# Kernel tuning notes

Measured on AMD Instinct MI355X. Metric: run time of the kernel, lower is better.

Reference implementation:

```python
import jax, jax.numpy as jnp
import numpy as np

N, IN_CH, HID, HEADS, NCLS, E = 50000, 128, 32, 8, 16, 800000
NEG_SLOPE = 0.2  # PyG GATConv default negative_slope


def setup_inputs() -> dict:
    key = jax.random.key(0)
    ks = jax.random.split(key, 10)
    sc = lambda fan: 1.0 / np.sqrt(fan).astype(np.float32)
    x = jax.random.normal(ks[0], (N, IN_CH), jnp.float32)
    edge_index = jax.random.randint(ks[1], (2, E), 0, N, jnp.int32)
    W1 = jax.random.normal(ks[2], (IN_CH, HEADS * HID), jnp.float32) * sc(IN_CH)
    att_src1 = jax.random.normal(ks[3], (HEADS, HID), jnp.float32) * sc(HID)
    att_dst1 = jax.random.normal(ks[4], (HEADS, HID), jnp.float32) * sc(HID)
    b1 = jnp.zeros((HEADS * HID,), jnp.float32)
    W2 = jax.random.normal(ks[5], (HEADS * HID, NCLS), jnp.float32) * sc(HEADS * HID)
    att_src2 = jax.random.normal(ks[6], (1, NCLS), jnp.float32) * sc(NCLS)
    att_dst2 = jax.random.normal(ks[7], (1, NCLS), jnp.float32) * sc(NCLS)
    b2 = jnp.zeros((NCLS,), jnp.float32)
    return {"x": x, "edge_index": edge_index, "W1": W1, "att_src1": att_src1,
            "att_dst1": att_dst1, "b1": b1, "W2": W2, "att_src2": att_src2,
            "att_dst2": att_dst2, "b2": b2}


def _gat_layer(x, W, a_src, a_dst, src, dst, heads, ch):
    """PyG GATConv core: per-edge LeakyReLU attention, scatter-softmax over
    destination neighborhoods, scatter-add aggregation. Returns [N, heads, ch]."""
    n = x.shape[0]
    h = (x @ W).reshape(n, heads, ch)                      # [N,H,C]
    e_src = jnp.einsum('nhc,hc->nh', h, a_src)             # [N,H]
    e_dst = jnp.einsum('nhc,hc->nh', h, a_dst)             # [N,H]
    e = jax.nn.leaky_relu(e_src[src] + e_dst[dst], NEG_SLOPE)  # [Etot,H]
    # scatter-softmax grouped by destination node (self-loops ensure nonempty)
    m = jax.ops.segment_max(e, dst, num_segments=n)        # [N,H]
    p = jnp.exp(e - m[dst])
    denom = jax.ops.segment_sum(p, dst, num_segments=n)    # [N,H]
    alpha = p / denom[dst]                                 # [Etot,H]
    out = jax.ops.segment_sum(alpha[:, :, None] * h[src], dst, num_segments=n)
    return out                                             # [N,H,C]


def reference(x, edge_index, W1, att_src1, att_dst1, b1, W2, att_src2, att_dst2, b2):
    n = x.shape[0]
    loops = jnp.arange(n, dtype=edge_index.dtype)          # add_self_loops=True
    src = jnp.concatenate([edge_index[0], loops])
    dst = jnp.concatenate([edge_index[1], loops])
    # conv1: heads=8, concat=True
    h1 = _gat_layer(x, W1, att_src1, att_dst1, src, dst, HEADS, HID)
    h1 = h1.reshape(n, HEADS * HID) + b1
    h1 = jax.nn.elu(h1)  # dropout is identity in eval mode
    # conv2: heads=1, concat=False (mean over 1 head == that head)
    h2 = _gat_layer(h1, W2, att_src2, att_dst2, src, dst, 1, NCLS)
    return h2[:, 0, :] + b2
```

## Files before the change

### kernel.cpp

```cpp
#include <hip/hip_runtime.h>
#include <hip/hip_bf16.h>


#define IN_CH 128
#define HIDC  256
#define NCLS  16
#define NEG_SLOPE 0.2f

typedef short bf16x8 __attribute__((ext_vector_type(8)));
typedef float f32x4 __attribute__((ext_vector_type(4)));

__device__ __forceinline__ unsigned int f2bf(float f) {
    unsigned int u = __float_as_uint(f);
    return (u + 0x7fffu + ((u >> 16) & 1u)) >> 16;
}
__device__ __forceinline__ float bf_lo(unsigned int w) { return __uint_as_float(w << 16); }
__device__ __forceinline__ float bf_hi(unsigned int w) { return __uint_as_float(w & 0xffff0000u); }


__global__ void count_fill_kernel(const int* __restrict__ ei, int* __restrict__ counts,
                                  int* __restrict__ erank, int E, int Etot,
                                  int* __restrict__ colB, int fill_n, int dummyB,
                                  unsigned short* __restrict__ Hb, float* __restrict__ ES1,
                                  float* __restrict__ H2, float* __restrict__ ES2,
                                  const float* __restrict__ W1,
                                  unsigned short* __restrict__ W1t, int N) {
    int i = blockIdx.x * blockDim.x + threadIdx.x;
    if (i < Etot) {
        int dst = (i < E) ? ei[E + i] : (i - E);
        erank[i] = atomicAdd(&counts[dst], 1);
    }
    if (i < fill_n) colB[i] = dummyB;
    if (i < IN_CH * HIDC) {
        int c = i >> 7, k = i & 127;
        W1t[i] = (unsigned short)f2bf(W1[k * HIDC + c]);
    }
    if (i < HIDC) Hb[(size_t)N * HIDC + i] = 0;
    if (i < NCLS) H2[(size_t)N * NCLS + i] = 0.f;
    if (i < 8) ES1[(size_t)N * 8 + i] = -3.0e38f;
    if (i == 0) ES2[N] = -3.0e38f;
}


__global__ __launch_bounds__(256) void scanA_kernel(const int* __restrict__ counts,
                                                    int* __restrict__ row_start,
                                                    int* __restrict__ bsums, int n) {
    __shared__ int wsum[4];
    int tid = threadIdx.x, lane = tid & 63, wid = tid >> 6;
    int i = blockIdx.x * 256 + tid;
    int v = (i < n) ? ((counts[i] + 3) & ~3) : 0;
    int x = v;
    #pragma unroll
    for (int off = 1; off < 64; off <<= 1) {
        int t = __shfl_up(x, off);
        if (lane >= off) x += t;
    }
    if (lane == 63) wsum[wid] = x;
    __syncthreads();
    if (tid < 4) {
        int w = wsum[tid];
        #pragma unroll
        for (int off = 1; off < 4; off <<= 1) {
            int t = __shfl_up(w, off);
            if (tid >= off) w += t;
        }
        wsum[tid] = w;
    }
    __syncthreads();
    int wex = wid ? wsum[wid - 1] : 0;
    if (i < n) row_start[i] = wex + (x - v);
    if (tid == 255) bsums[blockIdx.x] = wsum[3];
}

__global__ __launch_bounds__(256) void scanB_kernel(const int* __restrict__ bsums,
                                                    int* __restrict__ bofs,
                                                    int* __restrict__ row_start,
                                                    int nb, int n) {
    __shared__ int wsum[4];
    int tid = threadIdx.x, lane = tid & 63, wid = tid >> 6;
    int v = (tid < nb) ? bsums[tid] : 0;
    int x = v;
    #pragma unroll
    for (int off = 1; off < 64; off <<= 1) {
        int t = __shfl_up(x, off);
        if (lane >= off) x += t;
    }
    if (lane == 63) wsum[wid] = x;
    __syncthreads();
    if (tid < 4) {
        int w = wsum[tid];
        #pragma unroll
        for (int off = 1; off < 4; off <<= 1) {
            int t = __shfl_up(w, off);
            if (tid >= off) w += t;
        }
        wsum[tid] = w;
    }
    __syncthreads();
    int wex = wid ? wsum[wid - 1] : 0;
    if (tid < nb) bofs[tid] = wex + (x - v);
    if (tid == nb - 1) row_start[n] = wex + x;
}

__global__ __launch_bounds__(256) void scanC_kernel(int* __restrict__ row_start,
                                                    const int* __restrict__ bofs, int n) {
    int i = blockIdx.x * 256 + threadIdx.x;
    if (i < n) row_start[i] += bofs[blockIdx.x];
}

__global__ void scatter_kernel(const int* __restrict__ ei, const int* __restrict__ row_start,
                               const int* __restrict__ erank, int* __restrict__ colB,
                               int E, int Etot) {
    int e = blockIdx.x * blockDim.x + threadIdx.x;
    if (e >= Etot) return;
    int src, dst;
    if (e < E) { src = ei[e]; dst = ei[E + e]; }
    else       { src = e - E; dst = e - E; }
    colB[row_start[dst] + erank[e]] = src * (HIDC * 2);
}


#define LDK 72

__global__ __launch_bounds__(256) void gemm1_mfma(const float* __restrict__ A,
                                                  const unsigned short* __restrict__ W1t,
                                                  const float* __restrict__ a_src,
                                                  const float* __restrict__ a_dst,
                                                  unsigned short* __restrict__ Hb,
                                                  float* __restrict__ ES,
                                                  float* __restrict__ ED, int M) {
    __shared__ unsigned short As[128 * LDK];
    __shared__ unsigned short Bs[128 * LDK];
    int tid = threadIdx.x;
    int row0 = blockIdx.x * 128, col0 = blockIdx.y * 128;
    int lane = tid & 63, wid = tid >> 6;
    int wr = wid >> 1, wc = wid & 1;
    int la = lane & 15, lg = lane >> 4;
    f32x4 acc[4][4] = {};

    int r = tid >> 1, hf = tid & 1;
    int gr = row0 + r;
    bool okA = gr < M;
    const float4* asrc = reinterpret_cast<const float4*>(A + (size_t)(okA ? gr : 0) * IN_CH) + hf * 8;
    const uint4*  bsrc = reinterpret_cast<const uint4*>(W1t + (size_t)(col0 + r) * IN_CH) + hf * 4;
    unsigned short* adst = &As[r * LDK + hf * 32];
    unsigned short* bdst = &Bs[r * LDK + hf * 32];

    #pragma unroll
    for (int kt = 0; kt < 2; ++kt) {
        #pragma unroll
        for (int it = 0; it < 8; ++it) {
            float4 v = okA ? asrc[it] : make_float4(0.f, 0.f, 0.f, 0.f);
            uint2 w;
            w.x = f2bf(v.x) | (f2bf(v.y) << 16);
            w.y = f2bf(v.z) | (f2bf(v.w) << 16);
            *reinterpret_cast<uint2*>(adst + it * 4) = w;
        }
        #pragma unroll
        for (int it = 0; it < 4; ++it) {
            uint4 v = bsrc[it];
            *reinterpret_cast<uint4*>(bdst + it * 8) = v;
        }
        asrc += 16;
        bsrc += 8;
        __syncthreads();
        #pragma unroll
        for (int k0 = 0; k0 < 64; k0 += 32) {
            bf16x8 af[4], bfr[4];
            #pragma unroll
            for (int m = 0; m < 4; ++m)
                af[m] = *reinterpret_cast<const bf16x8*>(&As[(wr * 64 + m * 16 + la) * LDK + k0 + lg * 8]);
            #pragma unroll
            for (int n2 = 0; n2 < 4; ++n2)
                bfr[n2] = *reinterpret_cast<const bf16x8*>(&Bs[(wc * 64 + n2 * 16 + la) * LDK + k0 + lg * 8]);
            #pragma unroll
            for (int m = 0; m < 4; ++m) {
                #pragma unroll
                for (int n2 = 0; n2 < 4; ++n2)
                    acc[m][n2] = __builtin_amdgcn_mfma_f32_16x16x32_bf16(af[m], bfr[n2], acc[m][n2], 0, 0, 0);
            }
        }
        __syncthreads();
    }

    #pragma unroll
    for (int m = 0; m < 4; ++m) {
        #pragma unroll
        for (int j = 0; j < 4; ++j) {
            int grow = row0 + wr * 64 + m * 16 + lg * 4 + j;
            if (grow < M) {
                int gcol = col0 + wc * 64 + la;
                #pragma unroll
                for (int n2 = 0; n2 < 4; ++n2)
                    Hb[(size_t)grow * HIDC + gcol + n2 * 16] = (unsigned short)f2bf(acc[m][n2][j]);
            }
        }
    }

    int h0 = (col0 + wc * 64) >> 5;
    float as00 = a_src[h0 * 32 + la],        as01 = a_src[h0 * 32 + 16 + la];
    float ad00 = a_dst[h0 * 32 + la],        ad01 = a_dst[h0 * 32 + 16 + la];
    float as10 = a_src[(h0 + 1) * 32 + la],  as11 = a_src[(h0 + 1) * 32 + 16 + la];
    float ad10 = a_dst[(h0 + 1) * 32 + la],  ad11 = a_dst[(h0 + 1) * 32 + 16 + la];
    #pragma unroll
    for (int m = 0; m < 4; ++m) {
        #pragma unroll
        for (int j = 0; j < 4; ++j) {
            float v0 = acc[m][0][j], v1 = acc[m][1][j];
            float v2 = acc[m][2][j], v3 = acc[m][3][j];
            float es0 = v0 * as00 + v1 * as01;
            float ed0 = v0 * ad00 + v1 * ad01;
            float es1 = v2 * as10 + v3 * as11;
            float ed1 = v2 * ad10 + v3 * ad11;
            #pragma unroll
            for (int off = 1; off < 16; off <<= 1) {
                es0 += __shfl_xor(es0, off);
                ed0 += __shfl_xor(ed0, off);
                es1 += __shfl_xor(es1, off);
                ed1 += __shfl_xor(ed1, off);
            }
            int grow = row0 + wr * 64 + m * 16 + lg * 4 + j;
            if (la == 0 && grow < M) {
                ES[grow * 8 + h0] = es0;
                ED[grow * 8 + h0] = ed0;
                ES[grow * 8 + h0 + 1] = es1;
                ED[grow * 8 + h0 + 1] = ed1;
            }
        }
    }
}


#define EDGE4(cbv)                                                              \
    {                                                                           \
        float e0 = *(const float*)(ESb + (((cbv).x >> 4) | hoff));              \
        float e1 = *(const float*)(ESb + (((cbv).y >> 4) | hoff));              \
        float e2 = *(const float*)(ESb + (((cbv).z >> 4) | hoff));              \
        float e3 = *(const float*)(ESb + (((cbv).w >> 4) | hoff));              \
        uint2 v0 = *(const uint2*)(Hbb + ((cbv).x + lane8));                    \
        uint2 v1 = *(const uint2*)(Hbb + ((cbv).y + lane8));                    \
        uint2 v2 = *(const uint2*)(Hbb + ((cbv).z + lane8));                    \
        uint2 v3 = *(const uint2*)(Hbb + ((cbv).w + lane8));                    \
        e0 += ed; e1 += ed; e2 += ed; e3 += ed;                                 \
        e0 = fmaxf(e0, NEG_SLOPE * e0);                                         \
        e1 = fmaxf(e1, NEG_SLOPE * e1);                                         \
        e2 = fmaxf(e2, NEG_SLOPE * e2);                                         \
        e3 = fmaxf(e3, NEG_SLOPE * e3);                                         \
        float p0 = __expf(e0), p1 = __expf(e1), p2 = __expf(e2), p3 = __expf(e3);\
        s += (p0 + p1) + (p2 + p3);                                             \
        acc.x = fmaf(p0, bf_lo(v0.x), acc.x);                                   \
        acc.y = fmaf(p0, bf_hi(v0.x), acc.y);                                   \
        acc.z = fmaf(p0, bf_lo(v0.y), acc.z);                                   \
        acc.w = fmaf(p0, bf_hi(v0.y), acc.w);                                   \
        acc.x = fmaf(p1, bf_lo(v1.x), acc.x);                                   \
        acc.y = fmaf(p1, bf_hi(v1.x), acc.y);                                   \
        acc.z = fmaf(p1, bf_lo(v1.y), acc.z);                                   \
        acc.w = fmaf(p1, bf_hi(v1.y), acc.w);                                   \
        acc.x = fmaf(p2, bf_lo(v2.x), acc.x);                                   \
        acc.y = fmaf(p2, bf_hi(v2.x), acc.y);                                   \
        acc.z = fmaf(p2, bf_lo(v2.y), acc.z);                                   \
        acc.w = fmaf(p2, bf_hi(v2.y), acc.w);                                   \
        acc.x = fmaf(p3, bf_lo(v3.x), acc.x);                                   \
        acc.y = fmaf(p3, bf_hi(v3.x), acc.y);                                   \
        acc.z = fmaf(p3, bf_lo(v3.y), acc.z);                                   \
        acc.w = fmaf(p3, bf_hi(v3.y), acc.w);                                   \
    }

__global__ __launch_bounds__(256) void agg1_kernel(const unsigned short* __restrict__ Hb,
                                                   const float* __restrict__ ES,
                                                   const float* __restrict__ ED,
                                                   const int* __restrict__ row_start,
                                                   const int* __restrict__ colB,
                                                   const float* __restrict__ b1,
                                                   const float* __restrict__ W2,
                                                   const float* __restrict__ as2,
                                                   const float* __restrict__ ad2,
                                                   float* __restrict__ H2,
                                                   float* __restrict__ ES2,
                                                   float* __restrict__ ED2, int N) {
    __shared__ float W2t[16][260];
    __shared__ float h1row[4][260];
    int tid = threadIdx.x;
    #pragma unroll
    for (int it = 0; it < 16; ++it) {
        int idx = tid + it * 256;
        int c = idx & 15, k = idx >> 4;
        W2t[c][k + (k >> 6)] = W2[idx];
    }
    __syncthreads();

    int n = blockIdx.x * 4 + (tid >> 6);
    if (n >= N) return;
    int lane = tid & 63;
    int wv = tid >> 6;
    int h = lane >> 3;
    unsigned int hoff = h << 2;
    unsigned int lane8 = lane << 3;
    int s0 = row_start[n], s1 = row_start[n + 1];
    float ed = ED[n * 8 + h];
    const char* ESb = (const char*)ES;
    const char* Hbb = (const char*)Hb;

    float s = 0.f;
    float4 acc = make_float4(0.f, 0.f, 0.f, 0.f);

    int i = s0;
    for (; i + 7 < s1; i += 8) {
        uint4 cbA = *reinterpret_cast<const uint4*>(&colB[i]);
        uint4 cbB = *reinterpret_cast<const uint4*>(&colB[i + 4]);
        EDGE4(cbA);
        EDGE4(cbB);
    }
    if (i < s1) {
        uint4 cb = *reinterpret_cast<const uint4*>(&colB[i]);
        EDGE4(cb);
    }

    float inv = 1.0f / s;
    const float4 bv = *reinterpret_cast<const float4*>(&b1[lane * 4]);
    float4 o;
    o.x = acc.x * inv + bv.x;
    o.y = acc.y * inv + bv.y;
    o.z = acc.z * inv + bv.z;
    o.w = acc.w * inv + bv.w;
    o.x = o.x > 0.f ? o.x : expm1f(o.x);
    o.y = o.y > 0.f ? o.y : expm1f(o.y);
    o.z = o.z > 0.f ? o.z : expm1f(o.z);
    o.w = o.w > 0.f ? o.w : expm1f(o.w);

    {
        float* hr = &h1row[wv][0];
        int base = lane * 4 + (lane >> 4);
        hr[base + 0] = o.x;
        hr[base + 1] = o.y;
        hr[base + 2] = o.z;
        hr[base + 3] = o.w;
        __builtin_amdgcn_wave_barrier();
        int kg = lane >> 4, c = lane & 15;
        const float* wcol = &W2t[c][kg * 65];
        const float* hseg = &hr[kg * 65];
        float p = 0.f;
        #pragma unroll 16
        for (int k = 0; k < 64; ++k) p = fmaf(hseg[k], wcol[k], p);
        p += __shfl_xor(p, 16);
        p += __shfl_xor(p, 32);
        if (kg == 0) H2[(size_t)n * NCLS + c] = p;
        float es = p * as2[c];
        float edv = p * ad2[c];
        #pragma unroll
        for (int off = 1; off < 16; off <<= 1) {
            es += __shfl_xor(es, off);
            edv += __shfl_xor(edv, off);
        }
        if (lane == 0) {
            ES2[n] = es;
            ED2[n] = edv;
        }
    }
}


__global__ __launch_bounds__(256) void agg2_kernel(const float* __restrict__ H2,
                                                   const float* __restrict__ ES,
                                                   const float* __restrict__ ED,
                                                   const int* __restrict__ row_start,
                                                   const int* __restrict__ colB,
                                                   const float* __restrict__ b2,
                                                   float* __restrict__ out, int N) {
    int g = blockIdx.x * 4 + (threadIdx.x >> 6);
    if (g >= N) return;
    int lane = threadIdx.x & 63;
    int ep = lane >> 4;
    unsigned int c4 = (lane & 15) << 2;
    int s0 = row_start[g], s1 = row_start[g + 1];
    float ed = ED[g];
    const char* ESb = (const char*)ES;
    const char* H2b = (const char*)H2;
    float s = 0.f, acc = 0.f, sB = 0.f, accB = 0.f;
    int i = s0 + ep;
    for (; i + 4 < s1; i += 8) {
        unsigned int cb0 = (unsigned int)colB[i];
        unsigned int cb1 = (unsigned int)colB[i + 4];
        float e0 = *(const float*)(ESb + (cb0 >> 7));
        float e1 = *(const float*)(ESb + (cb1 >> 7));
        float hv0 = *(const float*)(H2b + ((cb0 >> 3) | c4));
        float hv1 = *(const float*)(H2b + ((cb1 >> 3) | c4));
        e0 += ed; e1 += ed;
        e0 = fmaxf(e0, NEG_SLOPE * e0);
        e1 = fmaxf(e1, NEG_SLOPE * e1);
        float p0 = __expf(e0), p1 = __expf(e1);
        s += p0; sB += p1;
        acc = fmaf(p0, hv0, acc);
        accB = fmaf(p1, hv1, accB);
    }
    if (i < s1) {
        unsigned int cb = (unsigned int)colB[i];
        float e = *(const float*)(ESb + (cb >> 7));
        float hv = *(const float*)(H2b + ((cb >> 3) | c4));
        e += ed;
        e = fmaxf(e, NEG_SLOPE * e);
        float p = __expf(e);
        s += p;
        acc = fmaf(p, hv, acc);
    }
    s += sB; acc += accB;
    s += __shfl_xor(s, 16);
    s += __shfl_xor(s, 32);
    acc += __shfl_xor(acc, 16);
    acc += __shfl_xor(acc, 32);
    if ((lane & 48) == 0) out[(size_t)g * NCLS + (lane & 15)] = acc / s + b2[lane & 15];
}


extern "C" void kernel_launch(void* const* d_in, const int* in_sizes, int n_in,
                              void* d_out, int out_size, void* d_ws, size_t ws_size,
                              hipStream_t stream) {
    const float* x   = (const float*)d_in[0];
    const int*   ei  = (const int*)d_in[1];
    const float* W1  = (const float*)d_in[2];
    const float* as1 = (const float*)d_in[3];
    const float* ad1 = (const float*)d_in[4];
    const float* b1  = (const float*)d_in[5];
    const float* W2  = (const float*)d_in[6];
    const float* as2 = (const float*)d_in[7];
    const float* ad2 = (const float*)d_in[8];
    const float* b2  = (const float*)d_in[9];
    float* out = (float*)d_out;

    int N = in_sizes[0] / IN_CH;
    int E = in_sizes[1] / 2;
    int Etot = E + N;
    int fill_n = E + 4 * N;
    int nb = (N + 255) / 256;

    char* ws = (char*)d_ws;
    size_t off = 0;
    auto alloc = [&](size_t bytes) -> void* {
        void* p = ws + off;
        off += (bytes + 255) & ~(size_t)255;
        return p;
    };
    unsigned short* Hb  = (unsigned short*)alloc((size_t)(N + 1) * HIDC * 2);
    unsigned short* W1t = (unsigned short*)alloc((size_t)HIDC * IN_CH * 2);
    float* H2  = (float*)alloc((size_t)(N + 1) * NCLS * 4);
    float* ES1 = (float*)alloc((size_t)(N + 1) * 8 * 4);
    float* ED1 = (float*)alloc((size_t)N * 8 * 4);
    float* ES2 = (float*)alloc((size_t)(N + 1) * 4);
    float* ED2 = (float*)alloc((size_t)N * 4);
    int* counts = (int*)alloc((size_t)N * 4);
    int* erank  = (int*)alloc((size_t)Etot * 4);
    int* row_start = (int*)alloc((size_t)(N + 1) * 4);
    int* colB = (int*)alloc((size_t)fill_n * 4);
    int* bsums = (int*)alloc((size_t)256 * 4);
    int* bofs  = (int*)alloc((size_t)256 * 4);

    hipMemsetAsync(counts, 0, (size_t)N * 4, stream);

    int eb = (Etot + 255) / 256;
    count_fill_kernel<<<(fill_n + 255) / 256, 256, 0, stream>>>(
        ei, counts, erank, E, Etot, colB, fill_n, N * HIDC * 2, Hb, ES1, H2, ES2, W1, W1t, N);
    scanA_kernel<<<nb, 256, 0, stream>>>(counts, row_start, bsums, N);
    scanB_kernel<<<1, 256, 0, stream>>>(bsums, bofs, row_start, nb, N);
    scanC_kernel<<<nb, 256, 0, stream>>>(row_start, bofs, N);
    scatter_kernel<<<eb, 256, 0, stream>>>(ei, row_start, erank, colB, E, Etot);

    dim3 g1((N + 127) / 128, 2);
    gemm1_mfma<<<g1, 256, 0, stream>>>(x, W1t, as1, ad1, Hb, ES1, ED1, N);
    agg1_kernel<<<(N + 3) / 4, 256, 0, stream>>>(Hb, ES1, ED1, row_start, colB, b1,
                                                 W2, as2, ad2, H2, ES2, ED2, N);
    agg2_kernel<<<(N + 3) / 4, 256, 0, stream>>>(H2, ES2, ED2, row_start, colB, b2, out, N);
}
```

Baseline: 276.1 us.

## Pack layer-2 features with source scores and drop shared-memory W2 staging

W2 is now transposed once into a global buffer in the fill kernel, which removes the per-block shared-memory load of W2 and its __syncthreads in agg1. The layer-2 projection is done with register float4 dot products and shuffle reductions. H2 and ES2 are interleaved into a 32-float padded row, so agg2 gathers each neighbor's score and features from the same cache line. The cost is doubled H2 row size and more shuffles per node in agg1.

```diff
diff --git a/kernel.cpp b/kernel.cpp
--- a/kernel.cpp
+++ b/kernel.cpp
@@ -22,9 +22,11 @@
                                   int* __restrict__ erank, int E, int Etot,
                                   int* __restrict__ colB, int fill_n, int dummyB,
                                   unsigned short* __restrict__ Hb, float* __restrict__ ES1,
-                                  float* __restrict__ H2, float* __restrict__ ES2,
+                                  float* __restrict__ H2p,
                                   const float* __restrict__ W1,
-                                  unsigned short* __restrict__ W1t, int N) {
+                                  unsigned short* __restrict__ W1t,
+                                  const float* __restrict__ W2,
+                                  float* __restrict__ W2t32, int N) {
     int i = blockIdx.x * blockDim.x + threadIdx.x;
     if (i < Etot) {
         int dst = (i < E) ? ei[E + i] : (i - E);
@@ -35,10 +37,13 @@
         int c = i >> 7, k = i & 127;
         W1t[i] = (unsigned short)f2bf(W1[k * HIDC + c]);
     }
+    if (i < HIDC * NCLS) {
+        int c = i >> 8, k = i & 255;
+        W2t32[i] = W2[k * NCLS + c];
+    }
     if (i < HIDC) Hb[(size_t)N * HIDC + i] = 0;
-    if (i < NCLS) H2[(size_t)N * NCLS + i] = 0.f;
+    if (i < 32) H2p[(size_t)N * 32 + i] = (i == 16) ? -3.0e38f : 0.f;
     if (i < 8) ES1[(size_t)N * 8 + i] = -3.0e38f;
-    if (i == 0) ES2[N] = -3.0e38f;
 }
 
 
@@ -272,27 +277,15 @@
                                                    const int* __restrict__ row_start,
                                                    const int* __restrict__ colB,
                                                    const float* __restrict__ b1,
-                                                   const float* __restrict__ W2,
+                                                   const float* __restrict__ W2t32,
                                                    const float* __restrict__ as2,
                                                    const float* __restrict__ ad2,
-                                                   float* __restrict__ H2,
-                                                   float* __restrict__ ES2,
+                                                   float* __restrict__ H2p,
                                                    float* __restrict__ ED2, int N) {
-    __shared__ float W2t[16][260];
-    __shared__ float h1row[4][260];
     int tid = threadIdx.x;
-    #pragma unroll
-    for (int it = 0; it < 16; ++it) {
-        int idx = tid + it * 256;
-        int c = idx & 15, k = idx >> 4;
-        W2t[c][k + (k >> 6)] = W2[idx];
-    }
-    __syncthreads();
-
     int n = blockIdx.x * 4 + (tid >> 6);
     if (n >= N) return;
     int lane = tid & 63;
-    int wv = tid >> 6;
     int h = lane >> 3;
     unsigned int hoff = h << 2;
     unsigned int lane8 = lane << 3;
@@ -329,40 +322,50 @@
     o.w = o.w > 0.f ? o.w : expm1f(o.w);
 
     {
-        float* hr = &h1row[wv][0];
-        int base = lane * 4 + (lane >> 4);
-        hr[base + 0] = o.x;
-        hr[base + 1] = o.y;
-        hr[base + 2] = o.z;
-        hr[base + 3] = o.w;
-        __builtin_amdgcn_wave_barrier();
-        int kg = lane >> 4, c = lane & 15;
-        const float* wcol = &W2t[c][kg * 65];
-        const float* hseg = &hr[kg * 65];
-        float p = 0.f;
-        #pragma unroll 16
-        for (int k = 0; k < 64; ++k) p = fmaf(hseg[k], wcol[k], p);
-        p += __shfl_xor(p, 16);
-        p += __shfl_xor(p, 32);
-        if (kg == 0) H2[(size_t)n * NCLS + c] = p;
-        float es = p * as2[c];
-        float edv = p * ad2[c];
-        #pragma unroll
-        for (int off = 1; off < 16; off <<= 1) {
-            es += __shfl_xor(es, off);
-            edv += __shfl_xor(edv, off);
+        const float4* w4 = reinterpret_cast<const float4*>(W2t32) + lane;
+        float p[16];
+        #pragma unroll
+        for (int c = 0; c < 16; ++c) {
+            float4 w = w4[c * 64];
+            p[c] = o.x * w.x + o.y * w.y + o.z * w.z + o.w * w.w;
+        }
+        #pragma unroll
+        for (int c = 0; c < 16; ++c) {
+            p[c] += __shfl_xor(p[c], 32);
+            p[c] += __shfl_xor(p[c], 16);
+        }
+        int q = lane >> 4;
+        float a0 = q < 2 ? (q == 0 ? p[0] : p[4])  : (q == 2 ? p[8]  : p[12]);
+        float a1 = q < 2 ? (q == 0 ? p[1] : p[5])  : (q == 2 ? p[9]  : p[13]);
+        float a2 = q < 2 ? (q == 0 ? p[2] : p[6])  : (q == 2 ? p[10] : p[14]);
+        float a3 = q < 2 ? (q == 0 ? p[3] : p[7])  : (q == 2 ? p[11] : p[15]);
+        #pragma unroll
+        for (int off = 8; off >= 1; off >>= 1) {
+            a0 += __shfl_xor(a0, off);
+            a1 += __shfl_xor(a1, off);
+            a2 += __shfl_xor(a2, off);
+            a3 += __shfl_xor(a3, off);
+        }
+        float4 asv = reinterpret_cast<const float4*>(as2)[q];
+        float4 adv = reinterpret_cast<const float4*>(ad2)[q];
+        float es  = a0 * asv.x + a1 * asv.y + a2 * asv.z + a3 * asv.w;
+        float edv = a0 * adv.x + a1 * adv.y + a2 * adv.z + a3 * adv.w;
+        es  += __shfl_xor(es, 16);  es  += __shfl_xor(es, 32);
+        edv += __shfl_xor(edv, 16); edv += __shfl_xor(edv, 32);
+        if ((lane & 15) == 0) {
+            float4 hv = make_float4(a0, a1, a2, a3);
+            *reinterpret_cast<float4*>(&H2p[(size_t)n * 32 + q * 4]) = hv;
         }
         if (lane == 0) {
-            ES2[n] = es;
+            H2p[(size_t)n * 32 + 16] = es;
             ED2[n] = edv;
         }
     }
 }
 
 
-__global__ __launch_bounds__(256) void agg2_kernel(const float* __restrict__ H2,
-                                                   const float* __restrict__ ES,
-                                                   const float* __restrict__ ED,
+__global__ __launch_bounds__(256) void agg2_kernel(const float* __restrict__ H2p,
+                                                   const float* __restrict__ ED2,
                                                    const int* __restrict__ row_start,
                                                    const int* __restrict__ colB,
                                                    const float* __restrict__ b2,
@@ -373,18 +376,17 @@
     int ep = lane >> 4;
     unsigned int c4 = (lane & 15) << 2;
     int s0 = row_start[g], s1 = row_start[g + 1];
-    float ed = ED[g];
-    const char* ESb = (const char*)ES;
-    const char* H2b = (const char*)H2;
+    float ed = ED2[g];
+    const char* H2b = (const char*)H2p;
     float s = 0.f, acc = 0.f, sB = 0.f, accB = 0.f;
     int i = s0 + ep;
     for (; i + 4 < s1; i += 8) {
-        unsigned int cb0 = (unsigned int)colB[i];
-        unsigned int cb1 = (unsigned int)colB[i + 4];
-        float e0 = *(const float*)(ESb + (cb0 >> 7));
-        float e1 = *(const float*)(ESb + (cb1 >> 7));
-        float hv0 = *(const float*)(H2b + ((cb0 >> 3) | c4));
-        float hv1 = *(const float*)(H2b + ((cb1 >> 3) | c4));
+        unsigned int r0 = ((unsigned int)colB[i]) >> 2;
+        unsigned int r1 = ((unsigned int)colB[i + 4]) >> 2;
+        float e0 = *(const float*)(H2b + (r0 | 64));
+        float e1 = *(const float*)(H2b + (r1 | 64));
+        float hv0 = *(const float*)(H2b + (r0 | c4));
+        float hv1 = *(const float*)(H2b + (r1 | c4));
         e0 += ed; e1 += ed;
         e0 = fmaxf(e0, NEG_SLOPE * e0);
         e1 = fmaxf(e1, NEG_SLOPE * e1);
@@ -394,9 +396,9 @@
         accB = fmaf(p1, hv1, accB);
     }
     if (i < s1) {
-        unsigned int cb = (unsigned int)colB[i];
-        float e = *(const float*)(ESb + (cb >> 7));
-        float hv = *(const float*)(H2b + ((cb >> 3) | c4));
+        unsigned int r = ((unsigned int)colB[i]) >> 2;
+        float e = *(const float*)(H2b + (r | 64));
+        float hv = *(const float*)(H2b + (r | c4));
         e += ed;
         e = fmaxf(e, NEG_SLOPE * e);
         float p = __expf(e);
@@ -440,12 +442,12 @@
         off += (bytes + 255) & ~(size_t)255;
         return p;
     };
-    unsigned short* Hb  = (unsigned short*)alloc((size_t)(N + 1) * HIDC * 2);
-    unsigned short* W1t = (unsigned short*)alloc((size_t)HIDC * IN_CH * 2);
-    float* H2  = (float*)alloc((size_t)(N + 1) * NCLS * 4);
+    unsigned short* Hb    = (unsigned short*)alloc((size_t)(N + 1) * HIDC * 2);
+    unsigned short* W1t   = (unsigned short*)alloc((size_t)HIDC * IN_CH * 2);
+    float*          W2t32 = (float*)alloc((size_t)HIDC * NCLS * 4);
+    float* H2p = (float*)alloc((size_t)(N + 1) * 32 * 4);
     float* ES1 = (float*)alloc((size_t)(N + 1) * 8 * 4);
     float* ED1 = (float*)alloc((size_t)N * 8 * 4);
-    float* ES2 = (float*)alloc((size_t)(N + 1) * 4);
     float* ED2 = (float*)alloc((size_t)N * 4);
     int* counts = (int*)alloc((size_t)N * 4);
     int* erank  = (int*)alloc((size_t)Etot * 4);
@@ -458,7 +460,8 @@
 
     int eb = (Etot + 255) / 256;
     count_fill_kernel<<<(fill_n + 255) / 256, 256, 0, stream>>>(
-        ei, counts, erank, E, Etot, colB, fill_n, N * HIDC * 2, Hb, ES1, H2, ES2, W1, W1t, N);
+        ei, counts, erank, E, Etot, colB, fill_n, N * HIDC * 2,
+        Hb, ES1, H2p, W1, W1t, W2, W2t32, N);
     scanA_kernel<<<nb, 256, 0, stream>>>(counts, row_start, bsums, N);
     scanB_kernel<<<1, 256, 0, stream>>>(bsums, bofs, row_start, nb, N);
     scanC_kernel<<<nb, 256, 0, stream>>>(row_start, bofs, N);
@@ -467,6 +470,6 @@
     dim3 g1((N + 127) / 128, 2);
     gemm1_mfma<<<g1, 256, 0, stream>>>(x, W1t, as1, ad1, Hb, ES1, ED1, N);
     agg1_kernel<<<(N + 3) / 4, 256, 0, stream>>>(Hb, ES1, ED1, row_start, colB, b1,
-                                                 W2, as2, ad2, H2, ES2, ED2, N);
-    agg2_kernel<<<(N + 3) / 4, 256, 0, stream>>>(H2, ES2, ED2, row_start, colB, b2, out, N);
-}
+                                                 W2t32, as2, ad2, H2p, ED2, N);
+    agg2_kernel<<<(N + 3) / 4, 256, 0, stream>>>(H2p, ED2, row_start, colB, b2, out, N);
+}
```

New measurement: 281.7 us. 1.02x slower.
